# Kernel tuning notes

Hardware: AMD Instinct MI355X
Metric: run time of the kernel (lower is better)

Reference implementation:

```python
import jax, jax.numpy as jnp
import numpy as np

B, S, H, NH = 2, 2048, 1024, 16
HD = H // NH


def setup_inputs() -> dict:
    key = jax.random.key(0)
    ks = jax.random.split(key, 12)
    inp = {
        "query": jax.random.normal(ks[0], (B, S, H), dtype=jnp.float32),
        "key": jax.random.normal(ks[1], (B, S, H), dtype=jnp.float32),
        "value": jax.random.normal(ks[2], (B, S, H), dtype=jnp.float32),
        "mask": jnp.ones((B, 1, S, S), dtype=jnp.int32),
        "script_mask": jax.random.uniform(ks[3], (B, S, S), dtype=jnp.float32),
    }
    scale = 1.0 / np.sqrt(H)
    inp["Wq"] = jax.random.normal(ks[4], (H, H), dtype=jnp.float32) * scale
    inp["bq"] = jnp.zeros((H,), dtype=jnp.float32)
    inp["Wk"] = jax.random.normal(ks[5], (H, H), dtype=jnp.float32) * scale
    inp["bk"] = jnp.zeros((H,), dtype=jnp.float32)
    inp["Wv"] = jax.random.normal(ks[6], (H, H), dtype=jnp.float32) * scale
    inp["bv"] = jnp.zeros((H,), dtype=jnp.float32)
    inp["Wo"] = jax.random.normal(ks[7], (H, H), dtype=jnp.float32) * scale
    inp["bo"] = jnp.zeros((H,), dtype=jnp.float32)
    return inp


def reference(query, key, value, mask, script_mask, Wq, bq, Wk, bk, Wv, bv, Wo, bo):
    b, s, h = query.shape
    # projections; torch Linear: x @ W.T + b
    q = (query @ Wq.T + bq).reshape(b, s, NH, HD).transpose(0, 2, 1, 3)  # [b,nh,s,hd]
    k = (key @ Wk.T + bk).reshape(b, s, NH, HD).transpose(0, 2, 1, 3)
    v = (value @ Wv.T + bv).reshape(b, s, NH, HD).transpose(0, 2, 1, 3)
    scores = jnp.einsum("bhqd,bhkd->bhqk", q, k) / jnp.sqrt(jnp.float32(HD))
    # multiplicative script mask, broadcast over heads
    scores = scores * script_mask[:, None, :, :]
    # additive mask: positions where mask == 0 -> -inf
    scores = jnp.where(mask == 0, -jnp.inf, scores)
    attn = jax.nn.softmax(scores, axis=-1)
    out = jnp.einsum("bhqk,bhkd->bhqd", attn, v)  # [b,nh,s,hd]
    out = out.transpose(0, 2, 1, 3).reshape(b, s, h)
    return out @ Wo.T + bo
```

## Files before the change

### kernel.cpp

```cpp
#include <hip/hip_runtime.h>
#include <stdint.h>

#define NH 16
#define SEQ 2048
#define HDIM 1024

typedef short bf16x8 __attribute__((ext_vector_type(8)));
typedef float f32x4 __attribute__((ext_vector_type(4)));

#define NEG_BIG (-1.0e30f)

static __device__ __forceinline__ uint32_t cvtpk_bf16(float lo, float hi) {
  uint32_t r;
  asm("v_cvt_pk_bf16_f32 %0, %1, %2" : "=v"(r) : "v"(lo), "v"(hi));
  return r;
}
static __device__ __forceinline__ uint16_t f2bf(float f) {
  return (uint16_t)cvtpk_bf16(f, f);
}
static __device__ __forceinline__ void gload_lds16(const void* g, void* l) {
  __builtin_amdgcn_global_load_lds(
      (const __attribute__((address_space(1))) void*)g,
      (__attribute__((address_space(3))) void*)l, 16, 0, 0);
}

struct CvtArgs {
  const float* src[7];
  uint16_t* dst[7];
  int nblk[7];
};
__global__ __launch_bounds__(256) void cvt_bf16(CvtArgs a) {
  int ten = blockIdx.y;
  if (blockIdx.x >= a.nblk[ten]) return;
  size_t idx = ((size_t)blockIdx.x * 256 + threadIdx.x) * 8;
  const float* s = a.src[ten] + idx;
  float4 f0 = *(const float4*)(s);
  float4 f1 = *(const float4*)(s + 4);
  uint4 o;
  o.x = cvtpk_bf16(f0.x, f0.y);
  o.y = cvtpk_bf16(f0.z, f0.w);
  o.z = cvtpk_bf16(f1.x, f1.y);
  o.w = cvtpk_bf16(f1.z, f1.w);
  *(uint4*)(a.dst[ten] + idx) = o;
}

__global__ __launch_bounds__(256) void cm_prep(const int4* __restrict__ mask,
                                               const float4* __restrict__ sm,
                                               uint4* __restrict__ cm) {
  int i = blockIdx.x * 256 + threadIdx.x;
  int4 m0 = mask[2 * i];
  int4 m1 = mask[2 * i + 1];
  float4 s0 = sm[2 * i];
  float4 s1 = sm[2 * i + 1];
  const float cst = 0.18033688011112042f;
  auto pk = [&](int mA, int mB, float fa, float fb) -> uint32_t {
    float a = mA ? fa * cst : -1.0f;
    float b = mB ? fb * cst : -1.0f;
    return cvtpk_bf16(a, b);
  };
  uint4 o;
  o.x = pk(m0.x, m0.y, s0.x, s0.y);
  o.y = pk(m0.z, m0.w, s0.z, s0.w);
  o.z = pk(m1.x, m1.y, s1.x, s1.y);
  o.w = pk(m1.z, m1.w, s1.z, s1.w);
  cm[i] = o;
}

struct GemmArgs {
  const uint16_t* A[4];
  const uint16_t* B[4];
  const float* bias[4];
  void* C[4];
};

__global__ __launch_bounds__(256) void gemm_bt(GemmArgs ga, int modeBase) {
  int mode = modeBase + blockIdx.y;
  const uint16_t* __restrict__ A = ga.A[mode];
  const uint16_t* __restrict__ Bm = ga.B[mode];
  const float* __restrict__ bias = ga.bias[mode];

  int bid = blockIdx.x;
  int tm, tn;
  if (mode == 2) { tm = bid & 7; tn = bid >> 3; }
  else           { tm = bid >> 3; tn = bid & 7; }

  __shared__ uint16_t As[3][128 * 32];
  __shared__ uint16_t Bs[3][128 * 32];

  int t = threadIdx.x;
  int lane = t & 63, w = t >> 6;
  int quad = lane >> 4, lm = lane & 15;
  int wm = w >> 1, wn = w & 1;

  const uint16_t* Ab = A + (size_t)tm * 128 * 1024;
  const uint16_t* Bb = Bm + (size_t)tn * 128 * 1024;

  int srow = lane >> 2;
  int scol = (lane & 3) * 8;
  const uint16_t* gA0 = Ab + (size_t)(w * 32 + srow) * 1024 + scol;
  const uint16_t* gA1 = gA0 + 16 * 1024;
  const uint16_t* gB0 = Bb + (size_t)(w * 32 + srow) * 1024 + scol;
  const uint16_t* gB1 = gB0 + 16 * 1024;

  uint16_t* rdA = As[0]; uint16_t* stA = As[1]; uint16_t* nxA = As[2];
  uint16_t* rdB = Bs[0]; uint16_t* stB = Bs[1]; uint16_t* nxB = Bs[2];
  int woff = w * 1024;

  auto STAGE = [&](uint16_t* dA, uint16_t* dB) {
    gload_lds16(gA0, dA + woff);
    gload_lds16(gA1, dA + woff + 512);
    gload_lds16(gB0, dB + woff);
    gload_lds16(gB1, dB + woff + 512);
    gA0 += 32; gA1 += 32; gB0 += 32; gB1 += 32;
  };

  f32x4 acc[4][4] = {};

  STAGE(rdA, rdB);

  for (int kk = 0; kk < 1024; kk += 32) {
    if (kk + 32 < 1024) {
      STAGE(stA, stB);
      asm volatile("s_waitcnt vmcnt(4)" ::: "memory");
    } else {
      asm volatile("s_waitcnt vmcnt(0)" ::: "memory");
    }
    __builtin_amdgcn_s_barrier();
    __builtin_amdgcn_sched_barrier(0);

    bf16x8 af[4], bfr[4];
#pragma unroll
    for (int i = 0; i < 4; i++)
      af[i] = *(const bf16x8*)&rdA[(wm * 64 + i * 16 + lm) * 32 + quad * 8];
#pragma unroll
    for (int j = 0; j < 4; j++)
      bfr[j] = *(const bf16x8*)&rdB[(wn * 64 + j * 16 + lm) * 32 + quad * 8];
#pragma unroll
    for (int i = 0; i < 4; i++)
#pragma unroll
      for (int j = 0; j < 4; j++)
        acc[i][j] = __builtin_amdgcn_mfma_f32_16x16x32_bf16(af[i], bfr[j], acc[i][j], 0, 0, 0);

    uint16_t* tA = rdA; rdA = stA; stA = nxA; nxA = tA;
    uint16_t* tB = rdB; rdB = stB; stB = nxB; nxB = tB;
  }

  int rowb = tm * 128 + wm * 64;
  int colb = tn * 128 + wn * 64;
#pragma unroll
  for (int i = 0; i < 4; i++) {
#pragma unroll
    for (int j = 0; j < 4; j++) {
      int col = colb + j * 16 + lm;
#pragma unroll
      for (int r = 0; r < 4; r++) {
        int row = rowb + i * 16 + quad * 4 + r;
        float v = acc[i][j][r];
        if (mode == 2) {
          v += bias[row];
          int hh = row >> 6, hd = row & 63, b = col >> 11, s2 = col & 2047;
          ((uint16_t*)ga.C[2])[((size_t)((b * NH + hh) * 64 + hd) << 11) + s2] = f2bf(v);
        } else {
          v += bias[col];
          int b = row >> 11, s2 = row & 2047, hh = col >> 6, hd = col & 63;
          ((uint16_t*)ga.C[mode])[(((size_t)(b * NH + hh) * 2048 + s2) << 6) + hd] = f2bf(v);
        }
      }
    }
  }
}

__global__ __launch_bounds__(256) void gemm_out(const uint16_t* __restrict__ A,
                                                const uint16_t* __restrict__ Bm,
                                                const float* __restrict__ bias,
                                                float* __restrict__ C) {
  int bid = blockIdx.x;
  int tm = bid >> 3;
  int tn = bid & 7;

  __shared__ uint16_t As[3][64 * 32];
  __shared__ uint16_t Bs[3][128 * 32];

  int t = threadIdx.x;
  int lane = t & 63, w = t >> 6;
  int quad = lane >> 4, lm = lane & 15;
  int wm = w >> 1, wn = w & 1;

  const uint16_t* Ab = A + (size_t)tm * 64 * 1024;
  const uint16_t* Bb = Bm + (size_t)tn * 128 * 1024;

  int srow = lane >> 2;
  int scol = (lane & 3) * 8;
  const uint16_t* gA0 = Ab + (size_t)(w * 16 + srow) * 1024 + scol;
  const uint16_t* gB0 = Bb + (size_t)(w * 32 + srow) * 1024 + scol;
  const uint16_t* gB1 = gB0 + 16 * 1024;

  uint16_t* rdA = As[0]; uint16_t* stA = As[1]; uint16_t* nxA = As[2];
  uint16_t* rdB = Bs[0]; uint16_t* stB = Bs[1]; uint16_t* nxB = Bs[2];
  int woffA = w * 512;
  int woffB = w * 1024;

  auto STAGE = [&](uint16_t* dA, uint16_t* dB) {
    gload_lds16(gA0, dA + woffA);
    gload_lds16(gB0, dB + woffB);
    gload_lds16(gB1, dB + woffB + 512);
    gA0 += 32; gB0 += 32; gB1 += 32;
  };

  f32x4 acc[2][4] = {};

  STAGE(rdA, rdB);

  for (int kk = 0; kk < 1024; kk += 32) {
    if (kk + 32 < 1024) {
      STAGE(stA, stB);
      asm volatile("s_waitcnt vmcnt(3)" ::: "memory");
    } else {
      asm volatile("s_waitcnt vmcnt(0)" ::: "memory");
    }
    __builtin_amdgcn_s_barrier();
    __builtin_amdgcn_sched_barrier(0);

    bf16x8 af[2], bfr[4];
#pragma unroll
    for (int i = 0; i < 2; i++)
      af[i] = *(const bf16x8*)&rdA[(wm * 32 + i * 16 + lm) * 32 + quad * 8];
#pragma unroll
    for (int j = 0; j < 4; j++)
      bfr[j] = *(const bf16x8*)&rdB[(wn * 64 + j * 16 + lm) * 32 + quad * 8];
#pragma unroll
    for (int i = 0; i < 2; i++)
#pragma unroll
      for (int j = 0; j < 4; j++)
        acc[i][j] = __builtin_amdgcn_mfma_f32_16x16x32_bf16(af[i], bfr[j], acc[i][j], 0, 0, 0);

    uint16_t* tA = rdA; rdA = stA; stA = nxA; nxA = tA;
    uint16_t* tB = rdB; rdB = stB; stB = nxB; nxB = tB;
  }

  int rowb = tm * 64 + wm * 32;
  int colb = tn * 128 + wn * 64;
#pragma unroll
  for (int i = 0; i < 2; i++) {
#pragma unroll
    for (int j = 0; j < 4; j++) {
      int col = colb + j * 16 + lm;
      float bv = bias[col];
#pragma unroll
      for (int r = 0; r < 4; r++) {
        int row = rowb + i * 16 + quad * 4 + r;
        C[(size_t)row * 1024 + col] = acc[i][j][r] + bv;
      }
    }
  }
}

#define LDK 72
#define KVBUF (64 * LDK)

__global__ __launch_bounds__(256) void attn(const uint16_t* __restrict__ qp,
                                            const uint16_t* __restrict__ kp,
                                            const uint16_t* __restrict__ vt,
                                            const uint16_t* __restrict__ cm,
                                            uint16_t* __restrict__ ao) {
  int h = blockIdx.x, qt = blockIdx.y, b = blockIdx.z;
  int t = threadIdx.x;
  int lane = t & 63, w = t >> 6;
  int quad = lane >> 4, c = lane & 15;

  __shared__ uint16_t Ks[2 * KVBUF];
  __shared__ uint16_t VTs[2 * KVBUF];
  __shared__ uint16_t Ps[KVBUF];

  size_t bh = (size_t)(b * NH + h);
  const uint16_t* Kb = kp + bh * (SEQ * 64);
  const uint16_t* Vb = vt + bh * (64 * SEQ);
  const uint16_t* CMb = cm + ((size_t)b * SEQ + qt * 64) * SEQ;

  int qrow = qt * 64 + w * 16 + c;
  const uint16_t* Qb = qp + bh * (SEQ * 64) + (size_t)qrow * 64;
  bf16x8 qf0 = *(const bf16x8*)(Qb + quad * 8);
  bf16x8 qf1 = *(const bf16x8*)(Qb + 32 + quad * 8);

  f32x4 Oacc[4] = {};
  float m_run = NEG_BIG;
  float l_run = 0.0f;

  int krow = w * 8 + (lane >> 3);
  int kc = (lane & 7) * 8;

  const uint16_t* pK0 = Kb + (size_t)krow * 64 + kc;
  const uint16_t* pK1 = pK0 + 32 * 64;
  const uint16_t* pV0 = Vb + (size_t)krow * SEQ + kc;
  const uint16_t* pV1 = pV0 + (size_t)32 * SEQ;
  const uint16_t* pCM = CMb + (size_t)(w * 16 + c) * SEQ + quad * 4;

  uint16_t* sK0 = &Ks[krow * LDK + kc];
  uint16_t* sK1 = sK0 + 32 * LDK;
  uint16_t* sV0 = &VTs[krow * LDK + kc];
  uint16_t* sV1 = sV0 + 32 * LDK;

  const uint16_t* rK = &Ks[c * LDK];
  const uint16_t* rV = &VTs[c * LDK];
  uint16_t* sP = &Ps[(w * 16 + c) * LDK];
  int qo = quad * 8;

  {
    uint4 k0  = *(const uint4*)(pK0);
    uint4 k1  = *(const uint4*)(pK1);
    uint4 v0g = *(const uint4*)(pV0);
    uint4 v1g = *(const uint4*)(pV1);
    pK0 += 64 * 64; pK1 += 64 * 64; pV0 += 64; pV1 += 64;
    *(uint4*)sK0 = k0;
    *(uint4*)sK1 = k1;
    *(uint4*)sV0 = v0g;
    *(uint4*)sV1 = v1g;
    asm volatile("s_waitcnt lgkmcnt(0)" ::: "memory");
    __builtin_amdgcn_s_barrier();
  }

  int X = 0;
  for (int kt = 0; kt < SEQ; kt += 64) {
    uint2 cm0 = *(const uint2*)(pCM);
    uint2 cm1 = *(const uint2*)(pCM + 16);
    uint2 cm2 = *(const uint2*)(pCM + 32);
    uint2 cm3 = *(const uint2*)(pCM + 48);
    pCM += 64;
    bool more = (kt + 64 < SEQ);
    uint4 k0, k1, v0g, v1g;
    if (more) {
      k0  = *(const uint4*)(pK0);
      k1  = *(const uint4*)(pK1);
      v0g = *(const uint4*)(pV0);
      v1g = *(const uint4*)(pV1);
      pK0 += 64 * 64; pK1 += 64 * 64; pV0 += 64; pV1 += 64;
    }

    const uint16_t* rKX = rK + X * KVBUF;
    const uint16_t* rVX = rV + X * KVBUF;

    f32x4 st[4];
    __builtin_amdgcn_s_setprio(1);
#pragma unroll
    for (int i = 0; i < 4; i++) {
      bf16x8 a0 = *(const bf16x8*)(rKX + i * 16 * LDK + qo);
      bf16x8 a1 = *(const bf16x8*)(rKX + i * 16 * LDK + 32 + qo);
      f32x4 z = {};
      z = __builtin_amdgcn_mfma_f32_16x16x32_bf16(a0, qf0, z, 0, 0, 0);
      st[i] = __builtin_amdgcn_mfma_f32_16x16x32_bf16(a1, qf1, z, 0, 0, 0);
    }
    __builtin_amdgcn_s_setprio(0);

    float p[16];
    float tmax = NEG_BIG;
    uint2 cmv[4] = {cm0, cm1, cm2, cm3};
#pragma unroll
    for (int i = 0; i < 4; i++) {
      uint32_t w0 = cmv[i].x, w1 = cmv[i].y;
      float cf[4];
      cf[0] = __builtin_bit_cast(float, w0 << 16);
      cf[1] = __builtin_bit_cast(float, w0 & 0xffff0000u);
      cf[2] = __builtin_bit_cast(float, w1 << 16);
      cf[3] = __builtin_bit_cast(float, w1 & 0xffff0000u);
#pragma unroll
      for (int r = 0; r < 4; r++) {
        float sv = st[i][r] * cf[r];
        sv = (cf[r] < 0.0f) ? NEG_BIG : sv;
        p[i * 4 + r] = sv;
      }
      tmax = fmaxf(tmax,
                   fmaxf(fmaxf(p[i * 4 + 0], p[i * 4 + 1]),
                         fmaxf(p[i * 4 + 2], p[i * 4 + 3])));
    }
    tmax = fmaxf(tmax, __shfl_xor(tmax, 16));
    tmax = fmaxf(tmax, __shfl_xor(tmax, 32));
    if (!__all(tmax <= m_run + 8.0f)) {
      float m_new = fmaxf(m_run, tmax);
      float alpha = exp2f(m_run - m_new);
      m_run = m_new;
      l_run *= alpha;
#pragma unroll
      for (int i = 0; i < 4; i++) Oacc[i] *= alpha;
    }
    float ls = 0.0f;
#pragma unroll
    for (int z2 = 0; z2 < 16; z2++) {
      p[z2] = exp2f(p[z2] - m_run);
      ls += p[z2];
    }
    l_run += ls;

#pragma unroll
    for (int i = 0; i < 4; i++) {
      uint2 pkd;
      pkd.x = cvtpk_bf16(p[i * 4 + 0], p[i * 4 + 1]);
      pkd.y = cvtpk_bf16(p[i * 4 + 2], p[i * 4 + 3]);
      *(uint2*)(sP + i * 16 + quad * 4) = pkd;
    }
    asm volatile("s_waitcnt lgkmcnt(0)" ::: "memory");
    __builtin_amdgcn_sched_barrier(0);

    bf16x8 pf0 = *(const bf16x8*)(sP + qo);
    bf16x8 pf1 = *(const bf16x8*)(sP + 32 + qo);
    __builtin_amdgcn_s_setprio(1);
#pragma unroll
    for (int i = 0; i < 4; i++) {
      bf16x8 v0 = *(const bf16x8*)(rVX + i * 16 * LDK + qo);
      bf16x8 v1 = *(const bf16x8*)(rVX + i * 16 * LDK + 32 + qo);
      Oacc[i] = __builtin_amdgcn_mfma_f32_16x16x32_bf16(v0, pf0, Oacc[i], 0, 0, 0);
      Oacc[i] = __builtin_amdgcn_mfma_f32_16x16x32_bf16(v1, pf1, Oacc[i], 0, 0, 0);
    }
    __builtin_amdgcn_s_setprio(0);

    if (more) {
      int Y = X ^ 1;
      *(uint4*)(sK0 + Y * KVBUF) = k0;
      *(uint4*)(sK1 + Y * KVBUF) = k1;
      *(uint4*)(sV0 + Y * KVBUF) = v0g;
      *(uint4*)(sV1 + Y * KVBUF) = v1g;
      asm volatile("s_waitcnt lgkmcnt(0)" ::: "memory");
      __builtin_amdgcn_s_barrier();
      X = Y;
    }
  }

  float lf = l_run + __shfl_xor(l_run, 16);
  lf = lf + __shfl_xor(lf, 32);
  float inv = 1.0f / lf;
  uint16_t* Ob = ao + ((size_t)(b * SEQ) + qt * 64 + w * 16 + c) * HDIM + h * 64;
#pragma unroll
  for (int i = 0; i < 4; i++) {
    uint2 ov;
    ov.x = cvtpk_bf16(Oacc[i][0] * inv, Oacc[i][1] * inv);
    ov.y = cvtpk_bf16(Oacc[i][2] * inv, Oacc[i][3] * inv);
    *(uint2*)(Ob + i * 16 + quad * 4) = ov;
  }
}

extern "C" void kernel_launch(void* const* d_in, const int* in_sizes, int n_in,
                              void* d_out, int out_size, void* d_ws, size_t ws_size,
                              hipStream_t stream) {
  (void)in_sizes; (void)n_in; (void)out_size; (void)ws_size;
  const float* query = (const float*)d_in[0];
  const float* key   = (const float*)d_in[1];
  const float* value = (const float*)d_in[2];
  const int*   mask  = (const int*)d_in[3];
  const float* smask = (const float*)d_in[4];
  const float* Wq = (const float*)d_in[5];
  const float* bq = (const float*)d_in[6];
  const float* Wk = (const float*)d_in[7];
  const float* bk = (const float*)d_in[8];
  const float* Wv = (const float*)d_in[9];
  const float* bv = (const float*)d_in[10];
  const float* Wo = (const float*)d_in[11];
  const float* bo = (const float*)d_in[12];

  char* p = (char*)d_ws;
  uint16_t* xq  = (uint16_t*)p; p += (size_t)2 * SEQ * HDIM * 2;
  uint16_t* xk  = (uint16_t*)p; p += (size_t)2 * SEQ * HDIM * 2;
  uint16_t* xv  = (uint16_t*)p; p += (size_t)2 * SEQ * HDIM * 2;
  uint16_t* wqb = (uint16_t*)p; p += (size_t)HDIM * HDIM * 2;
  uint16_t* wkb = (uint16_t*)p; p += (size_t)HDIM * HDIM * 2;
  uint16_t* wvb = (uint16_t*)p; p += (size_t)HDIM * HDIM * 2;
  uint16_t* wob = (uint16_t*)p; p += (size_t)HDIM * HDIM * 2;
  uint16_t* qp  = (uint16_t*)p; p += (size_t)2 * NH * SEQ * 64 * 2;
  uint16_t* kpp = (uint16_t*)p; p += (size_t)2 * NH * SEQ * 64 * 2;
  uint16_t* vtp = (uint16_t*)p; p += (size_t)2 * NH * SEQ * 64 * 2;
  uint16_t* cmw = (uint16_t*)p; p += (size_t)2 * SEQ * SEQ * 2;
  uint16_t* aob = (uint16_t*)p; p += (size_t)2 * SEQ * HDIM * 2;

  CvtArgs ca;
  ca.src[0] = query; ca.dst[0] = xq;  ca.nblk[0] = 2048;
  ca.src[1] = key;   ca.dst[1] = xk;  ca.nblk[1] = 2048;
  ca.src[2] = value; ca.dst[2] = xv;  ca.nblk[2] = 2048;
  ca.src[3] = Wq;    ca.dst[3] = wqb; ca.nblk[3] = 512;
  ca.src[4] = Wk;    ca.dst[4] = wkb; ca.nblk[4] = 512;
  ca.src[5] = Wv;    ca.dst[5] = wvb; ca.nblk[5] = 512;
  ca.src[6] = Wo;    ca.dst[6] = wob; ca.nblk[6] = 512;
  cvt_bf16<<<dim3(2048, 7), 256, 0, stream>>>(ca);

  cm_prep<<<4096, 256, 0, stream>>>((const int4*)mask, (const float4*)smask, (uint4*)cmw);

  GemmArgs ga;
  ga.A[0] = xq;  ga.B[0] = wqb; ga.bias[0] = bq; ga.C[0] = qp;
  ga.A[1] = xk;  ga.B[1] = wkb; ga.bias[1] = bk; ga.C[1] = kpp;
  ga.A[2] = wvb; ga.B[2] = xv;  ga.bias[2] = bv; ga.C[2] = vtp;
  ga.A[3] = aob; ga.B[3] = wob; ga.bias[3] = bo; ga.C[3] = d_out;

  gemm_bt<<<dim3(256, 3), 256, 0, stream>>>(ga, 0);
  attn<<<dim3(NH, SEQ / 64, 2), 256, 0, stream>>>(qp, kpp, vtp, cmw, aob);
  gemm_out<<<512, 256, 0, stream>>>(aob, wob, bo, (float*)d_out);
}
```

Before: 358.8 us.

## Merge conversion and mask prep kernels; single-buffer attention K/V tiles

Folds the bf16 conversion kernel and the combined-mask prep kernel into one launch with a flat grid that contains no idle blocks, which saves one launch and the early-exit blocks of the old 2D grid. The attention kernel drops the double-buffered K/V shared-memory tiles and instead loads each tile and stores it to LDS between two __syncthreads per iteration. This halves K/V LDS use, which may allow more resident blocks. In exchange it gives up overlapping the next tile's global loads with the current tile's compute and adds an extra barrier per iteration.

```diff
diff --git a/kernel.cpp b/kernel.cpp
--- a/kernel.cpp
+++ b/kernel.cpp
@@ -24,46 +24,48 @@
       (__attribute__((address_space(3))) void*)l, 16, 0, 0);
 }
 
-struct CvtArgs {
+struct PrepArgs {
   const float* src[7];
   uint16_t* dst[7];
-  int nblk[7];
+  const int4* mask;
+  const float4* sm;
+  uint4* cmw;
 };
-__global__ __launch_bounds__(256) void cvt_bf16(CvtArgs a) {
-  int ten = blockIdx.y;
-  if (blockIdx.x >= a.nblk[ten]) return;
-  size_t idx = ((size_t)blockIdx.x * 256 + threadIdx.x) * 8;
-  const float* s = a.src[ten] + idx;
-  float4 f0 = *(const float4*)(s);
-  float4 f1 = *(const float4*)(s + 4);
-  uint4 o;
-  o.x = cvtpk_bf16(f0.x, f0.y);
-  o.y = cvtpk_bf16(f0.z, f0.w);
-  o.z = cvtpk_bf16(f1.x, f1.y);
-  o.w = cvtpk_bf16(f1.z, f1.w);
-  *(uint4*)(a.dst[ten] + idx) = o;
-}
-
-__global__ __launch_bounds__(256) void cm_prep(const int4* __restrict__ mask,
-                                               const float4* __restrict__ sm,
-                                               uint4* __restrict__ cm) {
-  int i = blockIdx.x * 256 + threadIdx.x;
-  int4 m0 = mask[2 * i];
-  int4 m1 = mask[2 * i + 1];
-  float4 s0 = sm[2 * i];
-  float4 s1 = sm[2 * i + 1];
-  const float cst = 0.18033688011112042f;
-  auto pk = [&](int mA, int mB, float fa, float fb) -> uint32_t {
-    float a = mA ? fa * cst : -1.0f;
-    float b = mB ? fb * cst : -1.0f;
-    return cvtpk_bf16(a, b);
-  };
-  uint4 o;
-  o.x = pk(m0.x, m0.y, s0.x, s0.y);
-  o.y = pk(m0.z, m0.w, s0.z, s0.w);
-  o.z = pk(m1.x, m1.y, s1.x, s1.y);
-  o.w = pk(m1.z, m1.w, s1.z, s1.w);
-  cm[i] = o;
+__global__ __launch_bounds__(256) void prep(PrepArgs a) {
+  int x = blockIdx.x;
+  if (x < 8192) {
+    int ten, blk;
+    if (x < 6144) { ten = x >> 11; blk = x & 2047; }
+    else          { int y = x - 6144; ten = 3 + (y >> 9); blk = y & 511; }
+    size_t idx = ((size_t)blk * 256 + threadIdx.x) * 8;
+    const float* s = a.src[ten] + idx;
+    float4 f0 = *(const float4*)(s);
+    float4 f1 = *(const float4*)(s + 4);
+    uint4 o;
+    o.x = cvtpk_bf16(f0.x, f0.y);
+    o.y = cvtpk_bf16(f0.z, f0.w);
+    o.z = cvtpk_bf16(f1.x, f1.y);
+    o.w = cvtpk_bf16(f1.z, f1.w);
+    *(uint4*)(a.dst[ten] + idx) = o;
+  } else {
+    int i = (x - 8192) * 256 + threadIdx.x;
+    int4 m0 = a.mask[2 * i];
+    int4 m1 = a.mask[2 * i + 1];
+    float4 s0 = a.sm[2 * i];
+    float4 s1 = a.sm[2 * i + 1];
+    const float cst = 0.18033688011112042f;
+    auto pk = [&](int mA, int mB, float fa, float fb) -> uint32_t {
+      float va = mA ? fa * cst : -1.0f;
+      float vb = mB ? fb * cst : -1.0f;
+      return cvtpk_bf16(va, vb);
+    };
+    uint4 o;
+    o.x = pk(m0.x, m0.y, s0.x, s0.y);
+    o.y = pk(m0.z, m0.w, s0.z, s0.w);
+    o.z = pk(m1.x, m1.y, s1.x, s1.y);
+    o.w = pk(m1.z, m1.w, s1.z, s1.w);
+    a.cmw[i] = o;
+  }
 }
 
 struct GemmArgs {
@@ -256,7 +258,6 @@
 }
 
 #define LDK 72
-#define KVBUF (64 * LDK)
 
 __global__ __launch_bounds__(256) void attn(const uint16_t* __restrict__ qp,
                                             const uint16_t* __restrict__ kp,
@@ -268,9 +269,9 @@
   int lane = t & 63, w = t >> 6;
   int quad = lane >> 4, c = lane & 15;
 
-  __shared__ uint16_t Ks[2 * KVBUF];
-  __shared__ uint16_t VTs[2 * KVBUF];
-  __shared__ uint16_t Ps[KVBUF];
+  __shared__ uint16_t Ks[64 * LDK];
+  __shared__ uint16_t VTs[64 * LDK];
+  __shared__ uint16_t Ps[64 * LDK];
 
   size_t bh = (size_t)(b * NH + h);
   const uint16_t* Kb = kp + bh * (SEQ * 64);
@@ -305,46 +306,29 @@
   uint16_t* sP = &Ps[(w * 16 + c) * LDK];
   int qo = quad * 8;
 
-  {
-    uint4 k0  = *(const uint4*)(pK0);
-    uint4 k1  = *(const uint4*)(pK1);
-    uint4 v0g = *(const uint4*)(pV0);
-    uint4 v1g = *(const uint4*)(pV1);
-    pK0 += 64 * 64; pK1 += 64 * 64; pV0 += 64; pV1 += 64;
-    *(uint4*)sK0 = k0;
-    *(uint4*)sK1 = k1;
-    *(uint4*)sV0 = v0g;
-    *(uint4*)sV1 = v1g;
-    asm volatile("s_waitcnt lgkmcnt(0)" ::: "memory");
-    __builtin_amdgcn_s_barrier();
-  }
-
-  int X = 0;
   for (int kt = 0; kt < SEQ; kt += 64) {
     uint2 cm0 = *(const uint2*)(pCM);
     uint2 cm1 = *(const uint2*)(pCM + 16);
     uint2 cm2 = *(const uint2*)(pCM + 32);
     uint2 cm3 = *(const uint2*)(pCM + 48);
-    pCM += 64;
-    bool more = (kt + 64 < SEQ);
-    uint4 k0, k1, v0g, v1g;
-    if (more) {
-      k0  = *(const uint4*)(pK0);
-      k1  = *(const uint4*)(pK1);
-      v0g = *(const uint4*)(pV0);
-      v1g = *(const uint4*)(pV1);
-      pK0 += 64 * 64; pK1 += 64 * 64; pV0 += 64; pV1 += 64;
-    }
-
-    const uint16_t* rKX = rK + X * KVBUF;
-    const uint16_t* rVX = rV + X * KVBUF;
+    uint4 k0  = *(const uint4*)(pK0);
+    uint4 k1  = *(const uint4*)(pK1);
+    uint4 v0g = *(const uint4*)(pV0);
+    uint4 v1g = *(const uint4*)(pV1);
+    pCM += 64; pK0 += 64 * 64; pK1 += 64 * 64; pV0 += 64; pV1 += 64;
+    __syncthreads();
+    *(uint4*)sK0 = k0;
+    *(uint4*)sK1 = k1;
+    *(uint4*)sV0 = v0g;
+    *(uint4*)sV1 = v1g;
+    __syncthreads();
 
     f32x4 st[4];
     __builtin_amdgcn_s_setprio(1);
 #pragma unroll
     for (int i = 0; i < 4; i++) {
-      bf16x8 a0 = *(const bf16x8*)(rKX + i * 16 * LDK + qo);
-      bf16x8 a1 = *(const bf16x8*)(rKX + i * 16 * LDK + 32 + qo);
+      bf16x8 a0 = *(const bf16x8*)(rK + i * 16 * LDK + qo);
+      bf16x8 a1 = *(const bf16x8*)(rK + i * 16 * LDK + 32 + qo);
       f32x4 z = {};
       z = __builtin_amdgcn_mfma_f32_16x16x32_bf16(a0, qf0, z, 0, 0, 0);
       st[i] = __builtin_amdgcn_mfma_f32_16x16x32_bf16(a1, qf1, z, 0, 0, 0);
@@ -405,23 +389,12 @@
     __builtin_amdgcn_s_setprio(1);
 #pragma unroll
     for (int i = 0; i < 4; i++) {
-      bf16x8 v0 = *(const bf16x8*)(rVX + i * 16 * LDK + qo);
-      bf16x8 v1 = *(const bf16x8*)(rVX + i * 16 * LDK + 32 + qo);
+      bf16x8 v0 = *(const bf16x8*)(rV + i * 16 * LDK + qo);
+      bf16x8 v1 = *(const bf16x8*)(rV + i * 16 * LDK + 32 + qo);
       Oacc[i] = __builtin_amdgcn_mfma_f32_16x16x32_bf16(v0, pf0, Oacc[i], 0, 0, 0);
       Oacc[i] = __builtin_amdgcn_mfma_f32_16x16x32_bf16(v1, pf1, Oacc[i], 0, 0, 0);
     }
     __builtin_amdgcn_s_setprio(0);
-
-    if (more) {
-      int Y = X ^ 1;
-      *(uint4*)(sK0 + Y * KVBUF) = k0;
-      *(uint4*)(sK1 + Y * KVBUF) = k1;
-      *(uint4*)(sV0 + Y * KVBUF) = v0g;
-      *(uint4*)(sV1 + Y * KVBUF) = v1g;
-      asm volatile("s_waitcnt lgkmcnt(0)" ::: "memory");
-      __builtin_amdgcn_s_barrier();
-      X = Y;
-    }
   }
 
   float lf = l_run + __shfl_xor(l_run, 16);
@@ -469,17 +442,18 @@
   uint16_t* cmw = (uint16_t*)p; p += (size_t)2 * SEQ * SEQ * 2;
   uint16_t* aob = (uint16_t*)p; p += (size_t)2 * SEQ * HDIM * 2;
 
-  CvtArgs ca;
-  ca.src[0] = query; ca.dst[0] = xq;  ca.nblk[0] = 2048;
-  ca.src[1] = key;   ca.dst[1] = xk;  ca.nblk[1] = 2048;
-  ca.src[2] = value; ca.dst[2] = xv;  ca.nblk[2] = 2048;
-  ca.src[3] = Wq;    ca.dst[3] = wqb; ca.nblk[3] = 512;
-  ca.src[4] = Wk;    ca.dst[4] = wkb; ca.nblk[4] = 512;
-  ca.src[5] = Wv;    ca.dst[5] = wvb; ca.nblk[5] = 512;
-  ca.src[6] = Wo;    ca.dst[6] = wob; ca.nblk[6] = 512;
-  cvt_bf16<<<dim3(2048, 7), 256, 0, stream>>>(ca);
-
-  cm_prep<<<4096, 256, 0, stream>>>((const int4*)mask, (const float4*)smask, (uint4*)cmw);
+  PrepArgs pa;
+  pa.src[0] = query; pa.dst[0] = xq;
+  pa.src[1] = key;   pa.dst[1] = xk;
+  pa.src[2] = value; pa.dst[2] = xv;
+  pa.src[3] = Wq;    pa.dst[3] = wqb;
+  pa.src[4] = Wk;    pa.dst[4] = wkb;
+  pa.src[5] = Wv;    pa.dst[5] = wvb;
+  pa.src[6] = Wo;    pa.dst[6] = wob;
+  pa.mask = (const int4*)mask;
+  pa.sm   = (const float4*)smask;
+  pa.cmw  = (uint4*)cmw;
+  prep<<<12288, 256, 0, stream>>>(pa);
 
   GemmArgs ga;
   ga.A[0] = xq;  ga.B[0] = wqb; ga.bias[0] = bq; ga.C[0] = qp;
```

Result: faster. 330.6 us (-7.8%).
